# Performance work log

Measured on AMD Instinct MI355X. Metric: run time of the kernel, lower is better.

Reference implementation:

```python
import jax, jax.numpy as jnp
import numpy as np

BN_EPS = 1e-5


def conv1d_reflect(x, w, dilation, bias=None):
    # x: [N, C_in, L], w: [C_out, C_in, K]; reflect pad preserves length for K=3, pad=dilation
    k = w.shape[-1]
    p = ((k - 1) * dilation + 1) // 2
    xp = jnp.pad(x, ((0, 0), (0, 0), (p, p)), mode='reflect')
    y = jax.lax.conv_general_dilated(
        xp, w, window_strides=(1,), padding='VALID',
        rhs_dilation=(dilation,), dimension_numbers=('NCH', 'OIH', 'NCH'))
    if bias is not None:
        y = y + bias[None, :, None]
    return y


def bn_eval(x, gamma, beta, mean, var):
    inv = gamma / jnp.sqrt(var + BN_EPS)
    return x * inv[None, :, None] + (beta - mean * inv)[None, :, None]


def upsample2_linear(x):
    # F.interpolate(scale_factor=2, mode='linear', align_corners=False)
    L = x.shape[-1]
    src = (jnp.arange(2 * L, dtype=jnp.float32) + 0.5) * 0.5 - 0.5
    src = jnp.maximum(src, 0.0)
    i0 = jnp.floor(src).astype(jnp.int32)
    i1 = jnp.minimum(i0 + 1, L - 1)
    w = (src - i0.astype(jnp.float32)).astype(x.dtype)
    return x[..., i0] * (1.0 - w) + x[..., i1] * w


def setup_inputs() -> dict:
    key = jax.random.key(0)
    ks = jax.random.split(key, 6)
    bt, st, ch, nt = 16, 4, 512, 1024
    fusion = jax.random.normal(ks[0], (bt, st, ch, nt), dtype=jnp.float32)
    targets = jax.random.uniform(ks[1], (bt, 3, 4 * nt, st), dtype=jnp.float32)
    c1, c2 = 256, 32
    w1 = jax.random.normal(ks[2], (c1, ch, 3), dtype=jnp.float32) * 0.05
    w2 = jax.random.normal(ks[3], (c2, c1, 3), dtype=jnp.float32) * 0.05
    w_out = jax.random.normal(ks[4], (3, c2, 3), dtype=jnp.float32) * 0.05
    b_out = jnp.zeros((3,), dtype=jnp.float32)
    return {
        'fusion': fusion, 'targets': targets,
        'w1': w1,
        'bn1_gamma': jnp.ones((c1,), jnp.float32), 'bn1_beta': jnp.zeros((c1,), jnp.float32),
        'bn1_mean': jnp.zeros((c1,), jnp.float32), 'bn1_var': jnp.ones((c1,), jnp.float32),
        'w2': w2,
        'bn2_gamma': jnp.ones((c2,), jnp.float32), 'bn2_beta': jnp.zeros((c2,), jnp.float32),
        'bn2_mean': jnp.zeros((c2,), jnp.float32), 'bn2_var': jnp.ones((c2,), jnp.float32),
        'w_out': w_out, 'b_out': b_out,
    }


def reference(fusion, targets, w1, bn1_gamma, bn1_beta, bn1_mean, bn1_var,
              w2, bn2_gamma, bn2_beta, bn2_mean, bn2_var, w_out, b_out):
    bt, st, ch, nt = fusion.shape
    x = fusion.reshape(bt * st, ch, nt)
    x = jax.nn.relu(bn_eval(conv1d_reflect(x, w1, dilation=8), bn1_gamma, bn1_beta, bn1_mean, bn1_var))
    x = upsample2_linear(x)
    x = jax.nn.relu(bn_eval(conv1d_reflect(x, w2, dilation=16), bn2_gamma, bn2_beta, bn2_mean, bn2_var))
    x = upsample2_linear(x)
    x = conv1d_reflect(x, w_out, dilation=32, bias=b_out)
    x = x.reshape(bt, st, x.shape[1], x.shape[2])
    x = jnp.transpose(x, (0, 2, 3, 1))  # [bt, 3, 4*nt, st]

    # losses: vectorized masked CE (replaces the python double loop)
    logp = jax.nn.log_softmax(x.astype(jnp.float32), axis=1)
    valid = jnp.any(targets != 0, axis=(1, 2))  # [bt, st]
    num = jnp.sum(valid).astype(jnp.float32)
    T = targets.shape[2]
    loss = jnp.sum(-targets * logp) / (num * T)
    return x, loss
```

## Files before the change

### kernel.cpp

```cpp
#include <hip/hip_runtime.h>
#include <hip/hip_bf16.h>

#define DEV static __device__ __forceinline__

typedef short bf16x8_t __attribute__((ext_vector_type(8)));
typedef float f32x4 __attribute__((ext_vector_type(4)));

#define GLDS16(gp, lp) __builtin_amdgcn_global_load_lds( \
    (const __attribute__((address_space(1))) void*)(gp), \
    (__attribute__((address_space(3))) void*)(lp), 16, 0, 0)

DEV int reflect_idx(int q, int L) {
    q = q < 0 ? -q : q;
    q = q >= L ? 2 * L - 2 - q : q;
    return q;
}

DEV unsigned short f2bf(float f) {
    unsigned int b = __float_as_uint(f);
    unsigned int r = (b + 0x7FFFu + ((b >> 16) & 1u)) >> 16;
    return (unsigned short)r;
}
DEV float bf2f(unsigned short u) {
    return __uint_as_float(((unsigned int)u) << 16);
}

__global__ __launch_bounds__(256) void kprep_xt(
        const float* __restrict__ x, const float* __restrict__ w1,
        const float* __restrict__ w2, unsigned short* __restrict__ xb,
        unsigned short* __restrict__ wb, unsigned short* __restrict__ w2b,
        float* lacc, int n0) {
    const int tid = threadIdx.x;

    if (n0 == 0) {
        int bid = (blockIdx.z * gridDim.y + blockIdx.y) * gridDim.x + blockIdx.x;
        int g = bid * 256 + tid;
        if (g < 393216) {
            int kk = g >> 17;
            int rem = g & 131071;
            int co = rem >> 9;
            int ci = rem & 511;
            wb[g] = f2bf(w1[(co * 512 + ci) * 3 + kk]);
        } else if (g < 417792) {
            int j = g - 393216;
            int ci = j & 255;
            int co = (j >> 8) & 31;
            int kk = j >> 13;
            w2b[j] = f2bf(w2[(co * 256 + ci) * 3 + kk]);
        }
        if (g < 128) lacc[g] = 0.0f;
    }

    __shared__ float ls[64][65];
    const int t0 = blockIdx.x * 64, ci0 = blockIdx.y * 64;
    const int n = n0 + blockIdx.z;
    const float* xp = x + ((size_t)n * 512 + ci0) * 1024 + t0;

    float4 v[4];
#pragma unroll
    for (int i = 0; i < 4; ++i) {
        int idx = tid + i * 256;
        int r = idx >> 4, c4 = (idx & 15) * 4;
        v[i] = *(const float4*)(xp + r * 1024 + c4);
    }
#pragma unroll
    for (int i = 0; i < 4; ++i) {
        int idx = tid + i * 256;
        int r = idx >> 4, c4 = (idx & 15) * 4;
        ls[r][c4] = v[i].x; ls[r][c4 + 1] = v[i].y;
        ls[r][c4 + 2] = v[i].z; ls[r][c4 + 3] = v[i].w;
    }
    __syncthreads();
    unsigned short* xo = xb + ((size_t)blockIdx.z * 1024 + t0) * 512 + ci0;
#pragma unroll
    for (int p = 0; p < 2; ++p) {
        int trow = (tid >> 3) + p * 32;
        int cj = (tid & 7) * 8;
        unsigned short pk[8];
#pragma unroll
        for (int j = 0; j < 8; ++j) pk[j] = f2bf(ls[cj + j][trow]);
        *(uint4*)(xo + (size_t)trow * 512 + cj) = *(const uint4*)pk;
    }
}

__global__ __launch_bounds__(256, 4) void k1_mfma(
    const unsigned short* __restrict__ xb, const unsigned short* __restrict__ wb,
    const float* __restrict__ g, const float* __restrict__ be,
    const float* __restrict__ mn, const float* __restrict__ vr,
    unsigned short* __restrict__ y1t, int n0)
{
    const int tid  = threadIdx.x;
    const int lane = tid & 63;
    const int w    = tid >> 6;
    const int tw   = w >> 1;
    const int cw   = w & 1;
    const int tq   = lane & 15;
    const int qd   = lane >> 4;
    const int t0   = (blockIdx.x & 7) * 128;
    const int cb   = blockIdx.x >> 3;
    const int nr   = blockIdx.y;
    const int n    = n0 + nr;

    __shared__ unsigned short smem[17408];

    const int rl0 = tid >> 2;
    const int rl1 = 64 + (tid >> 2);
    const int q0  = (tid & 3) ^ ((rl0 >> 1) & 3);
    const int q1  = (tid & 3) ^ ((rl1 >> 1) & 3);

    const unsigned short* xn = xb + (size_t)nr * 1024 * 512;
    int aoff0[3], aoff1[3];
#pragma unroll
    for (int kk = 0; kk < 3; ++kk) {
        aoff0[kk] = reflect_idx(t0 + rl0 + 8 * kk - 8, 1024) * 512 + q0 * 8;
        aoff1[kk] = reflect_idx(t0 + rl1 + 8 * kk - 8, 1024) * 512 + q1 * 8;
    }
    const unsigned short* wp0 = wb + (size_t)(cb * 128 + rl0) * 512 + q0 * 8;
    const unsigned short* wp1 = wb + (size_t)(cb * 128 + rl1) * 512 + q1 * 8;

    const int atom = qd ^ ((tq >> 1) & 3);

    f32x4 acc[4][4];
#pragma unroll
    for (int a = 0; a < 4; ++a)
#pragma unroll
        for (int b = 0; b < 4; ++b) acc[a][b] = (f32x4){0.f, 0.f, 0.f, 0.f};

#define K1_ISSUE(i) do { \
    const int kk_ = (i) >> 4; const int col_ = ((i) & 15) * 32; \
    const int bo_ = ((i) & 1) * 8192; \
    GLDS16(xn + aoff0[kk_] + col_, &smem[bo_ + tid * 8]); \
    GLDS16(xn + aoff1[kk_] + col_, &smem[bo_ + 2048 + tid * 8]); \
    GLDS16(wp0 + (size_t)kk_ * 131072 + col_, &smem[bo_ + 4096 + tid * 8]); \
    GLDS16(wp1 + (size_t)kk_ * 131072 + col_, &smem[bo_ + 6144 + tid * 8]); \
} while (0)

    K1_ISSUE(0);

#pragma unroll
    for (int c = 0; c < 48; ++c) {
        __syncthreads();
        if (c < 47) K1_ISSUE(c + 1);
        const int ab = (c & 1) * 8192;
        bf16x8_t Af[4], Bf[4];
#pragma unroll
        for (int ts = 0; ts < 4; ++ts)
            Af[ts] = *(const bf16x8_t*)&smem[ab + (tw * 64 + ts * 16 + tq) * 32 + atom * 8];
#pragma unroll
        for (int cs = 0; cs < 4; ++cs)
            Bf[cs] = *(const bf16x8_t*)&smem[ab + 4096 + (cw * 64 + cs * 16 + tq) * 32 + atom * 8];
#pragma unroll
        for (int ts = 0; ts < 4; ++ts)
#pragma unroll
            for (int cs = 0; cs < 4; ++cs)
                acc[ts][cs] = __builtin_amdgcn_mfma_f32_16x16x32_bf16(
                    Af[ts], Bf[cs], acc[ts][cs], 0, 0, 0);
    }
#undef K1_ISSUE

    __syncthreads();
#pragma unroll
    for (int cs = 0; cs < 4; ++cs) {
        int col = cw * 64 + cs * 16 + tq;
        int co  = cb * 128 + col;
        float iv = g[co] / sqrtf(vr[co] + 1e-5f);
        float sh = be[co] - mn[co] * iv;
#pragma unroll
        for (int ts = 0; ts < 4; ++ts)
#pragma unroll
            for (int rg = 0; rg < 4; ++rg)
                smem[(tw * 64 + ts * 16 + qd * 4 + rg) * 136 + col] =
                    f2bf(fmaxf(fmaf(acc[ts][cs][rg], iv, sh), 0.0f));
    }
    __syncthreads();
    const int srow = tid >> 4, sseg = tid & 15;
#pragma unroll
    for (int p = 0; p < 8; ++p) {
        int row = p * 16 + srow;
        unsigned short* yp = y1t + ((size_t)n * 1024 + t0 + row) * 256 + cb * 128 + sseg * 8;
        *(uint4*)yp = *(const uint4*)&smem[row * 136 + sseg * 8];
    }
}

__global__ __launch_bounds__(256, 2) void k2_mfma(
    const unsigned short* __restrict__ y1t, const unsigned short* __restrict__ w2b,
    const float* __restrict__ g, const float* __restrict__ be,
    const float* __restrict__ mn, const float* __restrict__ vr,
    float* __restrict__ y2t)
{
    const int tid  = threadIdx.x;
    const int lane = tid & 63;
    const int w    = tid >> 6;
    const int tq   = lane & 15;
    const int qd   = lane >> 4;
    const int t0   = blockIdx.x * 256;
    const int n    = blockIdx.y;

    __shared__ union SM {
        unsigned short us[2][288 * 40];
        float tr[256 * 36];
    } sm;

    f32x4 acc[4][2];
#pragma unroll
    for (int a = 0; a < 4; ++a)
#pragma unroll
        for (int b = 0; b < 2; ++b) acc[a][b] = (f32x4){0.f, 0.f, 0.f, 0.f};

    const unsigned short* yn = y1t + (size_t)n * 1024 * 256;

    auto stage = [&](int ch, int buf) {
        const int ci0 = ch * 32;
        for (int idx = tid; idx < 1152; idx += 256) {
            int r = idx >> 2, gq = idx & 3;
            int u = reflect_idx(t0 - 16 + r, 2048);
            float src = fmaxf((float)u * 0.5f - 0.25f, 0.0f);
            int i0 = (int)src;
            float wl = src - (float)i0;
            int i1 = i0 + 1 > 1023 ? 1023 : i0 + 1;
            const unsigned short* p0 = yn + (size_t)i0 * 256 + ci0 + gq * 8;
            const unsigned short* p1 = yn + (size_t)i1 * 256 + ci0 + gq * 8;
            uint4 ua = *(const uint4*)p0;
            uint4 ub = *(const uint4*)p1;
            const unsigned short* sa = (const unsigned short*)&ua;
            const unsigned short* sb = (const unsigned short*)&ub;
            unsigned short pk[8];
#pragma unroll
            for (int j = 0; j < 8; ++j) {
                float a = bf2f(sa[j]);
                float b = bf2f(sb[j]);
                pk[j] = f2bf(a + wl * (b - a));
            }
            *(uint4*)&sm.us[buf][r * 40 + gq * 8] = *(const uint4*)pk;
        }
    };

    stage(0, 0);
    for (int ch = 0; ch < 8; ++ch) {
        const int buf = ch & 1;
        __syncthreads();
        if (ch < 7) stage(ch + 1, buf ^ 1);

        const int ci0 = ch * 32;
        bf16x8_t Bf[2][3];
#pragma unroll
        for (int cs = 0; cs < 2; ++cs)
#pragma unroll
            for (int kk = 0; kk < 3; ++kk)
                Bf[cs][kk] = *(const bf16x8_t*)(w2b +
                    ((size_t)(kk * 32 + cs * 16 + tq)) * 256 + ci0 + qd * 8);

        bf16x8_t Af[6];
#pragma unroll
        for (int s = 0; s < 6; ++s)
            Af[s] = *(const bf16x8_t*)&sm.us[buf][(w * 64 + s * 16 + tq) * 40 + qd * 8];

#pragma unroll
        for (int ts = 0; ts < 4; ++ts)
#pragma unroll
            for (int cs = 0; cs < 2; ++cs)
#pragma unroll
                for (int kk = 0; kk < 3; ++kk)
                    acc[ts][cs] = __builtin_amdgcn_mfma_f32_16x16x32_bf16(
                        Af[ts + kk], Bf[cs][kk], acc[ts][cs], 0, 0, 0);
    }

    __syncthreads();
#pragma unroll
    for (int cs = 0; cs < 2; ++cs) {
        int co = cs * 16 + tq;
        float iv = g[co] / sqrtf(vr[co] + 1e-5f);
        float sh = be[co] - mn[co] * iv;
#pragma unroll
        for (int ts = 0; ts < 4; ++ts)
#pragma unroll
            for (int rg = 0; rg < 4; ++rg) {
                int tl = w * 64 + ts * 16 + qd * 4 + rg;
                sm.tr[tl * 36 + co] = fmaxf(fmaf(acc[ts][cs][rg], iv, sh), 0.0f);
            }
    }
    __syncthreads();
    float* yo = y2t + ((size_t)n * 2048 + t0 + tid) * 32;
#pragma unroll
    for (int j = 0; j < 8; ++j)
        *(float4*)(yo + j * 4) = *(const float4*)&sm.tr[tid * 36 + j * 4];
}

__global__ __launch_bounds__(256, 2) void k3_ce(
    const float* __restrict__ y2t, const float* __restrict__ w3,
    const float* __restrict__ bias, const float* __restrict__ tg,
    float* __restrict__ out, float* lacc)
{
    const int tid = threadIdx.x;
    const int t0 = blockIdx.x * 256;
    const int n  = blockIdx.y;

    __shared__ float us[32 * 321];
    __shared__ float wsh[288];
    __shared__ float wsum[4];
    __shared__ int snz[4];

    for (int idx = tid; idx < 288; idx += 256) wsh[idx] = w3[idx];

    const float* yn = y2t + (size_t)n * 2048 * 32;
    for (int idx = tid; idx < 1280; idx += 256) {
        int r = idx >> 2, gq = idx & 3;
        int u = reflect_idx(t0 - 32 + r, 4096);
        float src = fmaxf((float)u * 0.5f - 0.25f, 0.0f);
        int i0 = (int)src;
        float wl = src - (float)i0;
        int i1 = i0 + 1 > 2047 ? 2047 : i0 + 1;
        const float* p0 = yn + (size_t)i0 * 32 + gq * 8;
        const float* p1 = yn + (size_t)i1 * 32 + gq * 8;
        float4 a0 = *(const float4*)p0;
        float4 a1 = *(const float4*)(p0 + 4);
        float4 b0 = *(const float4*)p1;
        float4 b1 = *(const float4*)(p1 + 4);
        float v[8];
        v[0] = a0.x + wl * (b0.x - a0.x); v[1] = a0.y + wl * (b0.y - a0.y);
        v[2] = a0.z + wl * (b0.z - a0.z); v[3] = a0.w + wl * (b0.w - a0.w);
        v[4] = a1.x + wl * (b1.x - a1.x); v[5] = a1.y + wl * (b1.y - a1.y);
        v[6] = a1.z + wl * (b1.z - a1.z); v[7] = a1.w + wl * (b1.w - a1.w);
#pragma unroll
        for (int j = 0; j < 8; ++j)
            us[(gq * 8 + j) * 321 + r] = v[j];
    }
    __syncthreads();

    float a0 = 0.0f, a1 = 0.0f, a2 = 0.0f;
#pragma unroll 8
    for (int ci = 0; ci < 32; ++ci) {
        float x0 = us[ci * 321 + tid];
        float x1 = us[ci * 321 + tid + 32];
        float x2 = us[ci * 321 + tid + 64];
        a0 = fmaf(wsh[(0 * 32 + ci) * 3 + 0], x0, a0);
        a0 = fmaf(wsh[(0 * 32 + ci) * 3 + 1], x1, a0);
        a0 = fmaf(wsh[(0 * 32 + ci) * 3 + 2], x2, a0);
        a1 = fmaf(wsh[(1 * 32 + ci) * 3 + 0], x0, a1);
        a1 = fmaf(wsh[(1 * 32 + ci) * 3 + 1], x1, a1);
        a1 = fmaf(wsh[(1 * 32 + ci) * 3 + 2], x2, a1);
        a2 = fmaf(wsh[(2 * 32 + ci) * 3 + 0], x0, a2);
        a2 = fmaf(wsh[(2 * 32 + ci) * 3 + 1], x1, a2);
        a2 = fmaf(wsh[(2 * 32 + ci) * 3 + 2], x2, a2);
    }
    int b = n >> 2, s = n & 3;
    int t = t0 + tid;
    size_t ob = ((size_t)(b * 3) * 4096 + t) * 4 + s;
    float x0 = a0 + bias[0];
    float x1 = a1 + bias[1];
    float x2 = a2 + bias[2];
    out[ob]         = x0;
    out[ob + 16384] = x1;
    out[ob + 32768] = x2;

    float mx = fmaxf(x0, fmaxf(x1, x2));
    float e0 = expf(x0 - mx), e1 = expf(x1 - mx), e2 = expf(x2 - mx);
    float lse = mx + logf(e0 + e1 + e2);
    float g0 = tg[ob], g1 = tg[ob + 16384], g2 = tg[ob + 32768];
    float v = g0 * (lse - x0) + g1 * (lse - x1) + g2 * (lse - x2);
    bool nz = (g0 != 0.0f) | (g1 != 0.0f) | (g2 != 0.0f);

    for (int off = 32; off > 0; off >>= 1) v += __shfl_down(v, off);
    unsigned long long m = __ballot(nz);
    int lane = tid & 63, wid = tid >> 6;
    if (lane == 0) { wsum[wid] = v; snz[wid] = (m != 0ull); }
    __syncthreads();
    if (tid == 0) {
        atomicAdd(lacc, wsum[0] + wsum[1] + wsum[2] + wsum[3]);
        if (snz[0] | snz[1] | snz[2] | snz[3])
            atomicOr((int*)lacc + 8 + n, 1);
    }
}

__global__ void k4c_final(const float* lacc, float* out) {
    if (threadIdx.x == 0) {
        float sum = lacc[0];
        const int* vf = (const int*)lacc + 8;
        int num = 0;
#pragma unroll
        for (int j = 0; j < 64; ++j) num += (vf[j] != 0);
        out[786432] = sum / ((float)num * 4096.0f);
    }
}

extern "C" void kernel_launch(void* const* d_in, const int* in_sizes, int n_in,
                              void* d_out, int out_size, void* d_ws, size_t ws_size,
                              hipStream_t stream) {
    (void)in_sizes; (void)n_in; (void)out_size;
    const float* fusion  = (const float*)d_in[0];
    const float* targets = (const float*)d_in[1];
    const float* w1  = (const float*)d_in[2];
    const float* g1  = (const float*)d_in[3];
    const float* be1 = (const float*)d_in[4];
    const float* mn1 = (const float*)d_in[5];
    const float* vr1 = (const float*)d_in[6];
    const float* w2  = (const float*)d_in[7];
    const float* g2  = (const float*)d_in[8];
    const float* be2 = (const float*)d_in[9];
    const float* mn2 = (const float*)d_in[10];
    const float* vr2 = (const float*)d_in[11];
    const float* w3  = (const float*)d_in[12];
    const float* b3  = (const float*)d_in[13];
    float* out = (float*)d_out;

    char* ws = (char*)d_ws;
    unsigned short* y1t = (unsigned short*)ws;
    unsigned short* xb  = (unsigned short*)(ws + 33554432);
    float* y2t = (float*)(ws + 33554432);

    const bool single = ws_size >= 101500000ull;
    size_t woff = single ? (33554432ull + 67108864ull) : (33554432ull + 16777216ull);
    unsigned short* wb  = (unsigned short*)(ws + woff);
    unsigned short* w2b = (unsigned short*)(ws + woff + 786432);
    float* lacc = (float*)(ws + woff + 786432 + 49152);

    if (single) {
        kprep_xt<<<dim3(16, 8, 64), 256, 0, stream>>>(fusion, w1, w2, xb, wb, w2b, lacc, 0);
        k1_mfma<<<dim3(16, 64), 256, 0, stream>>>(xb, wb, g1, be1, mn1, vr1, y1t, 0);
    } else {
        for (int r = 0; r < 4; ++r) {
            kprep_xt<<<dim3(16, 8, 16), 256, 0, stream>>>(fusion, w1, w2, xb, wb, w2b, lacc, r * 16);
            k1_mfma<<<dim3(16, 16), 256, 0, stream>>>(xb, wb, g1, be1, mn1, vr1, y1t, r * 16);
        }
    }
    k2_mfma<<<dim3(8, 64), 256, 0, stream>>>(y1t, w2b, g2, be2, mn2, vr2, y2t);
    k3_ce<<<dim3(16, 64), 256, 0, stream>>>(y2t, w3, b3, targets, out, lacc);
    k4c_final<<<1, 64, 0, stream>>>(lacc, out);
}
```

Measured before the change: 342.8 us.

## Reuse staged activation rows across the three dilated conv taps in conv1

Reorders the conv1 K-loop from tap-major to channel-chunk-major. Each 32-channel chunk of the input now loads one 144-row activation tile into LDS, and all three dilation-8 taps read it at row offsets of 8·tap. Before, each tap loaded its own 128-row tile. This cuts global-to-LDS traffic for activations by roughly two-thirds. In exchange the activation and weight buffers get separate double-buffer schedules. A third partial row group is loaded by only one wavefront, which adds slight load imbalance.

```diff
diff --git a/kernel.cpp b/kernel.cpp
--- a/kernel.cpp
+++ b/kernel.cpp
@@ -107,17 +107,18 @@
     const int rl1 = 64 + (tid >> 2);
     const int q0  = (tid & 3) ^ ((rl0 >> 1) & 3);
     const int q1  = (tid & 3) ^ ((rl1 >> 1) & 3);
-
-    const unsigned short* xn = xb + (size_t)nr * 1024 * 512;
-    int aoff0[3], aoff1[3];
-#pragma unroll
-    for (int kk = 0; kk < 3; ++kk) {
-        aoff0[kk] = reflect_idx(t0 + rl0 + 8 * kk - 8, 1024) * 512 + q0 * 8;
-        aoff1[kk] = reflect_idx(t0 + rl1 + 8 * kk - 8, 1024) * 512 + q1 * 8;
-    }
     const unsigned short* wp0 = wb + (size_t)(cb * 128 + rl0) * 512 + q0 * 8;
     const unsigned short* wp1 = wb + (size_t)(cb * 128 + rl1) * 512 + q1 * 8;
 
+    const unsigned short* xn = xb + (size_t)nr * 1024 * 512;
+    const int qA = (tid & 3) ^ ((tid >> 3) & 3);
+    int arA[3];
+#pragma unroll
+    for (int rd = 0; rd < 3; ++rd) {
+        int r = rd * 64 + (tid >> 2);
+        arA[rd] = reflect_idx(t0 + r - 8, 1024) * 512 + qA * 8;
+    }
+
     const int atom = qd ^ ((tq >> 1) & 3);
 
     f32x4 acc[4][4];
@@ -126,29 +127,38 @@
 #pragma unroll
         for (int b = 0; b < 4; ++b) acc[a][b] = (f32x4){0.f, 0.f, 0.f, 0.f};
 
-#define K1_ISSUE(i) do { \
-    const int kk_ = (i) >> 4; const int col_ = ((i) & 15) * 32; \
-    const int bo_ = ((i) & 1) * 8192; \
-    GLDS16(xn + aoff0[kk_] + col_, &smem[bo_ + tid * 8]); \
-    GLDS16(xn + aoff1[kk_] + col_, &smem[bo_ + 2048 + tid * 8]); \
-    GLDS16(wp0 + (size_t)kk_ * 131072 + col_, &smem[bo_ + 4096 + tid * 8]); \
-    GLDS16(wp1 + (size_t)kk_ * 131072 + col_, &smem[bo_ + 6144 + tid * 8]); \
+#define K1A(ch) do { \
+    const int ao_ = ((ch) & 1) * 4608; \
+    GLDS16(xn + arA[0] + (ch) * 32, &smem[ao_ + tid * 8]); \
+    GLDS16(xn + arA[1] + (ch) * 32, &smem[ao_ + 2048 + tid * 8]); \
+    if (tid < 64) GLDS16(xn + arA[2] + (ch) * 32, &smem[ao_ + 4096 + tid * 8]); \
 } while (0)
 
-    K1_ISSUE(0);
+#define K1B(i) do { \
+    const int kk_ = (i) % 3; const int ch_ = (i) / 3; \
+    const int bo_ = 9216 + ((i) & 1) * 4096; \
+    GLDS16(wp0 + (size_t)kk_ * 131072 + ch_ * 32, &smem[bo_ + tid * 8]); \
+    GLDS16(wp1 + (size_t)kk_ * 131072 + ch_ * 32, &smem[bo_ + 2048 + tid * 8]); \
+} while (0)
+
+    K1A(0);
+    K1B(0);
 
 #pragma unroll
     for (int c = 0; c < 48; ++c) {
         __syncthreads();
-        if (c < 47) K1_ISSUE(c + 1);
-        const int ab = (c & 1) * 8192;
+        if (c < 47) K1B(c + 1);
+        if ((c % 3) == 2 && c < 45) K1A(c / 3 + 1);
+        const int kk = c % 3;
+        const int ab = ((c / 3) & 1) * 4608;
+        const int bb = 9216 + (c & 1) * 4096;
         bf16x8_t Af[4], Bf[4];
 #pragma unroll
         for (int ts = 0; ts < 4; ++ts)
-            Af[ts] = *(const bf16x8_t*)&smem[ab + (tw * 64 + ts * 16 + tq) * 32 + atom * 8];
+            Af[ts] = *(const bf16x8_t*)&smem[ab + (tw * 64 + ts * 16 + tq + 8 * kk) * 32 + atom * 8];
 #pragma unroll
         for (int cs = 0; cs < 4; ++cs)
-            Bf[cs] = *(const bf16x8_t*)&smem[ab + 4096 + (cw * 64 + cs * 16 + tq) * 32 + atom * 8];
+            Bf[cs] = *(const bf16x8_t*)&smem[bb + (cw * 64 + cs * 16 + tq) * 32 + atom * 8];
 #pragma unroll
         for (int ts = 0; ts < 4; ++ts)
 #pragma unroll
@@ -156,7 +166,8 @@
                 acc[ts][cs] = __builtin_amdgcn_mfma_f32_16x16x32_bf16(
                     Af[ts], Bf[cs], acc[ts][cs], 0, 0, 0);
     }
-#undef K1_ISSUE
+#undef K1A
+#undef K1B
 
     __syncthreads();
 #pragma unroll
```

New measurement: 333.5 us. 2.7% less time.
